# Performance work log

Measured on AMD Instinct MI355X. Metric: run time of the kernel, lower is better.

The kernel has to match this reference:

```python
import jax, jax.numpy as jnp
import numpy as np
from jax import lax

B, S, W = 64, 64, 12          # batch, sentences, words-per-sentence (max_seq)
V, SYM, HID = 32000, 128, 256  # vocab, symbol_size, hidden_size
E, R = 64, 32                  # entity_size, role_size
EPS = 1e-5


def _mlp(x, W1, b1, W2, b2):
    # equation 'b...e,er->b...r' is a matmul on the last axis; tanh hidden, linear out
    return jnp.tanh(x @ W1 + b1) @ W2 + b2


def _ln(x, g, b):
    mu = jnp.mean(x, axis=-1, keepdims=True)
    var = jnp.mean(jnp.square(x - mu), axis=-1, keepdims=True)
    return (x - mu) * lax.rsqrt(var + EPS) * g + b


def setup_inputs() -> dict:
    key = jax.random.key(0)
    ks = jax.random.split(key, 24)
    s_in = 1.0 / np.sqrt(SYM)
    s_h = 1.0 / np.sqrt(HID)
    inp = {
        "story": jax.random.randint(ks[0], (B, S, W), 0, V),
        "query": jax.random.randint(ks[1], (B, W), 0, V),
        "word_embed": jax.random.uniform(ks[2], (V, SYM), jnp.float32, -0.1, 0.1),
        "pos_embed": jnp.ones((W, SYM), jnp.float32) / W,
        # UpdateModule MLPs: 2 entity heads (out=E), 3 role heads (out=R), stacked
        "ue_W1": jax.random.normal(ks[3], (2, SYM, HID)) * s_in,
        "ue_b1": jnp.zeros((2, HID), jnp.float32),
        "ue_W2": jax.random.normal(ks[4], (2, HID, E)) * s_h,
        "ue_b2": jnp.zeros((2, E), jnp.float32),
        "ur_W1": jax.random.normal(ks[5], (3, SYM, HID)) * s_in,
        "ur_b1": jnp.zeros((3, HID), jnp.float32),
        "ur_W2": jax.random.normal(ks[6], (3, HID, R)) * s_h,
        "ur_b2": jnp.zeros((3, R), jnp.float32),
        # InferenceModule MLPs
        "ie_W1": jax.random.normal(ks[7], (2, SYM, HID)) * s_in,
        "ie_b1": jnp.zeros((2, HID), jnp.float32),
        "ie_W2": jax.random.normal(ks[8], (2, HID, E)) * s_h,
        "ie_b2": jnp.zeros((2, E), jnp.float32),
        "ir_W1": jax.random.normal(ks[9], (3, SYM, HID)) * s_in,
        "ir_b1": jnp.zeros((3, HID), jnp.float32),
        "ir_W2": jax.random.normal(ks[10], (3, HID, R)) * s_h,
        "ir_b2": jnp.zeros((3, R), jnp.float32),
        "ln_g": jnp.ones((3, E), jnp.float32),
        "ln_b": jnp.zeros((3, E), jnp.float32),
        "Z": jax.random.normal(ks[11], (E, V)) * (1.0 / np.sqrt(E)),
    }
    return inp


def reference(story, query, word_embed, pos_embed,
              ue_W1, ue_b1, ue_W2, ue_b2, ur_W1, ur_b1, ur_W2, ur_b2,
              ie_W1, ie_b1, ie_W2, ie_b2, ir_W1, ir_b1, ir_W2, ir_b2,
              ln_g, ln_b, Z):
    # ---- InputModule ----
    sent = jnp.einsum('bswe,we->bse', word_embed[story], pos_embed)   # [B,S,SYM]
    qsum = jnp.einsum('bwe,we->be', word_embed[query], pos_embed)     # [B,SYM]

    # ---- UpdateModule: precompute per-step entity/role vectors ----
    e1 = _mlp(sent, ue_W1[0], ue_b1[0], ue_W2[0], ue_b2[0])  # [B,S,E]
    e2 = _mlp(sent, ue_W1[1], ue_b1[1], ue_W2[1], ue_b2[1])
    r1 = _mlp(sent, ur_W1[0], ur_b1[0], ur_W2[0], ur_b2[0])  # [B,S,R]
    r2 = _mlp(sent, ur_W1[1], ur_b1[1], ur_W2[1], ur_b2[1])
    r3 = _mlp(sent, ur_W1[2], ur_b1[2], ur_W2[2], ur_b2[2])
    paW = jnp.einsum('bsr,bsf->bsrf', r1, e2)
    paB = jnp.einsum('bsr,bsf->bsrf', r3, e1)

    xs = tuple(jnp.moveaxis(t, 1, 0) for t in (e1, r1, paW, e2, r2, paB, r3))

    def step(TPR, x):
        e1i, r1i, paWi, e2i, r2i, paBi, r3i = x
        t1 = jnp.einsum('be,berf->brf', e1i, TPR)
        w_hat = jnp.einsum('br,brf->bf', r1i, t1)
        m_hat = jnp.einsum('br,brf->bf', r2i, t1)
        b_hat = jnp.einsum('be,br,berf->bf', e2i, r3i, TPR)
        write_op = paWi - r1i[:, :, None] * w_hat[:, None, :]
        move_op = r2i[:, :, None] * (w_hat - m_hat)[:, None, :]
        back_op = paBi - r3i[:, :, None] * b_hat[:, None, :]
        delta = (jnp.einsum('be,brf->berf', e1i, write_op + move_op)
                 + jnp.einsum('be,brf->berf', e2i, back_op))
        return TPR + delta, None

    TPR0 = jnp.zeros((sent.shape[0], E, R, E), sent.dtype)
    TPR, _ = lax.scan(step, TPR0, xs)

    # ---- InferenceModule ----
    qe1 = _mlp(qsum, ie_W1[0], ie_b1[0], ie_W2[0], ie_b2[0])
    qr1 = _mlp(qsum, ir_W1[0], ir_b1[0], ir_W2[0], ir_b2[0])
    qr2 = _mlp(qsum, ir_W1[1], ir_b1[1], ir_W2[1], ir_b2[1])
    qr3 = _mlp(qsum, ir_W1[2], ir_b1[2], ir_W2[2], ir_b2[2])
    i1 = _ln(jnp.einsum('be,br,berf->bf', qe1, qr1, TPR), ln_g[0], ln_b[0])
    i2 = _ln(jnp.einsum('be,br,berf->bf', i1, qr2, TPR), ln_g[1], ln_b[1])
    i3 = _ln(jnp.einsum('be,br,berf->bf', i2, qr3, TPR), ln_g[2], ln_b[2])
    return (i1 + i2 + i3) @ Z
```

## Files before the change

### kernel.cpp

```cpp
#include <hip/hip_runtime.h>
#include <math.h>

#define B_   64
#define S_   64
#define W_   12
#define V_   32000
#define SYM_ 128
#define HID_ 256
#define E_   64
#define R_   32

__global__ __launch_bounds__(128) void k_embed(
    const int* __restrict__ story, const int* __restrict__ query,
    const float* __restrict__ we, const float* __restrict__ pe,
    float* __restrict__ X) {
  int row = blockIdx.x;
  int e = threadIdx.x;
  const int* idx = (row < 4096) ? story + row * W_ : query + (row - 4096) * W_;
  float acc = 0.f;
#pragma unroll
  for (int w = 0; w < W_; ++w)
    acc = fmaf(we[(long)idx[w] * SYM_ + e], pe[w * SYM_ + e], acc);
  X[row * SYM_ + e] = acc;
}

__global__ __launch_bounds__(256) void k_mlp(
    const float* __restrict__ X,
    const float* __restrict__ ueW1, const float* __restrict__ ueb1,
    const float* __restrict__ ueW2, const float* __restrict__ ueb2,
    const float* __restrict__ urW1, const float* __restrict__ urb1,
    const float* __restrict__ urW2, const float* __restrict__ urb2,
    const float* __restrict__ ieW1, const float* __restrict__ ieb1,
    const float* __restrict__ ieW2, const float* __restrict__ ieb2,
    const float* __restrict__ irW1, const float* __restrict__ irb1,
    const float* __restrict__ irW2, const float* __restrict__ irb2,
    float* __restrict__ oE0, float* __restrict__ oE1,
    float* __restrict__ oR0, float* __restrict__ oR1, float* __restrict__ oR2) {
  __shared__ float SM[8320];

  int h = blockIdx.x % 5;
  int tile = blockIdx.x / 5;
  int rowbase = tile * 32;
  bool isQ = (rowbase >= 4096);
  bool isE = (h < 2);
  const float* W1 = isE ? (isQ ? ieW1 : ueW1) + h * (SYM_ * HID_)
                        : (isQ ? irW1 : urW1) + (h - 2) * (SYM_ * HID_);
  const float* b1 = isE ? (isQ ? ieb1 : ueb1) + h * HID_
                        : (isQ ? irb1 : urb1) + (h - 2) * HID_;
  const float* W2 = isE ? (isQ ? ieW2 : ueW2) + h * (HID_ * E_)
                        : (isQ ? irW2 : urW2) + (h - 2) * (HID_ * R_);
  const float* b2 = isE ? (isQ ? ieb2 : ueb2) + h * E_
                        : (isQ ? irb2 : urb2) + (h - 2) * R_;
  float* out = (h == 0) ? oE0 : (h == 1) ? oE1 : (h == 2) ? oR0 : (h == 3) ? oR1 : oR2;

  int tid = threadIdx.x;
  int wv = tid >> 6;
  int l = tid & 63;

#pragma unroll
  for (int c = 0; c < 4; ++c) {
    int i = tid + 256 * c;
    int row = i >> 5, k4 = (i & 31) * 4;
    *(float4*)&SM[row * 136 + k4] = *(const float4*)(X + (long)(rowbase + row) * SYM_ + k4);
  }
  __syncthreads();

  float a[8][4];
#pragma unroll
  for (int i = 0; i < 8; ++i)
#pragma unroll
    for (int q = 0; q < 4; ++q) a[i][q] = 0.f;

  const float* W1p = W1 + 4 * l;
#pragma unroll 2
  for (int kg = 0; kg < 32; ++kg) {
    float4 w0 = *(const float4*)(W1p + (long)(4 * kg + 0) * HID_);
    float4 w1 = *(const float4*)(W1p + (long)(4 * kg + 1) * HID_);
    float4 w2 = *(const float4*)(W1p + (long)(4 * kg + 2) * HID_);
    float4 w3 = *(const float4*)(W1p + (long)(4 * kg + 3) * HID_);
    float4 xr[8];
#pragma unroll
    for (int i = 0; i < 8; ++i)
      xr[i] = *(const float4*)&SM[(8 * wv + i) * 136 + 4 * kg];
#pragma unroll
    for (int i = 0; i < 8; ++i) {
      a[i][0] = fmaf(xr[i].x, w0.x, a[i][0]);
      a[i][1] = fmaf(xr[i].x, w0.y, a[i][1]);
      a[i][2] = fmaf(xr[i].x, w0.z, a[i][2]);
      a[i][3] = fmaf(xr[i].x, w0.w, a[i][3]);
      a[i][0] = fmaf(xr[i].y, w1.x, a[i][0]);
      a[i][1] = fmaf(xr[i].y, w1.y, a[i][1]);
      a[i][2] = fmaf(xr[i].y, w1.z, a[i][2]);
      a[i][3] = fmaf(xr[i].y, w1.w, a[i][3]);
      a[i][0] = fmaf(xr[i].z, w2.x, a[i][0]);
      a[i][1] = fmaf(xr[i].z, w2.y, a[i][1]);
      a[i][2] = fmaf(xr[i].z, w2.z, a[i][2]);
      a[i][3] = fmaf(xr[i].z, w2.w, a[i][3]);
      a[i][0] = fmaf(xr[i].w, w3.x, a[i][0]);
      a[i][1] = fmaf(xr[i].w, w3.y, a[i][1]);
      a[i][2] = fmaf(xr[i].w, w3.z, a[i][2]);
      a[i][3] = fmaf(xr[i].w, w3.w, a[i][3]);
    }
  }
  __syncthreads();
  {
    float4 b1v = *(const float4*)(b1 + 4 * l);
#pragma unroll
    for (int i = 0; i < 8; ++i) {
      float4 hv = make_float4(tanhf(a[i][0] + b1v.x), tanhf(a[i][1] + b1v.y),
                              tanhf(a[i][2] + b1v.z), tanhf(a[i][3] + b1v.w));
      *(float4*)&SM[(8 * wv + i) * 260 + 4 * l] = hv;
    }
  }
  __syncthreads();
  if (isE) {
    float acc[8];
#pragma unroll
    for (int i = 0; i < 8; ++i) acc[i] = 0.f;
#pragma unroll 2
    for (int c4 = 0; c4 < 64; ++c4) {
      float w0 = W2[(long)(4 * c4 + 0) * E_ + l];
      float w1 = W2[(long)(4 * c4 + 1) * E_ + l];
      float w2 = W2[(long)(4 * c4 + 2) * E_ + l];
      float w3 = W2[(long)(4 * c4 + 3) * E_ + l];
#pragma unroll
      for (int i = 0; i < 8; ++i) {
        float4 hh = *(const float4*)&SM[(8 * wv + i) * 260 + 4 * c4];
        acc[i] = fmaf(hh.x, w0, fmaf(hh.y, w1, fmaf(hh.z, w2, fmaf(hh.w, w3, acc[i]))));
      }
    }
    float bb = b2[l];
#pragma unroll
    for (int i = 0; i < 8; ++i)
      out[(long)(rowbase + 8 * wv + i) * E_ + l] = acc[i] + bb;
  } else {
    int lc = l & 31;
    float acc[8];
#pragma unroll
    for (int i = 0; i < 8; ++i) acc[i] = 0.f;
#pragma unroll 2
    for (int c4 = 0; c4 < 64; ++c4) {
      float w0 = W2[(long)(4 * c4 + 0) * R_ + lc];
      float w1 = W2[(long)(4 * c4 + 1) * R_ + lc];
      float w2 = W2[(long)(4 * c4 + 2) * R_ + lc];
      float w3 = W2[(long)(4 * c4 + 3) * R_ + lc];
#pragma unroll
      for (int i = 0; i < 8; ++i) {
        float4 hh = *(const float4*)&SM[(8 * wv + i) * 260 + 4 * c4];
        acc[i] = fmaf(hh.x, w0, fmaf(hh.y, w1, fmaf(hh.z, w2, fmaf(hh.w, w3, acc[i]))));
      }
    }
    if (l < 32) {
      float bb = b2[lc];
#pragma unroll
      for (int i = 0; i < 8; ++i)
        out[(long)(rowbase + 8 * wv + i) * R_ + lc] = acc[i] + bb;
    }
  }
}

__global__ __launch_bounds__(256) void k_gram(
    const float* __restrict__ e1, const float* __restrict__ e2,
    const float* __restrict__ r1, const float* __restrict__ r2,
    const float* __restrict__ r3, float* __restrict__ Wt) {
  int b = blockIdx.x / 9, m = blockIdx.x % 9;
  const float* sE = ((m < 6) ? e1 : e2) + (long)b * S_ * E_;
  const float* jE = ((m == 2 || m == 5 || m == 8) ? e2 : e1) + (long)b * S_ * E_;
  int sk = m / 3, jk = m % 3;
  const float* sR = ((sk == 0) ? r1 : (sk == 1) ? r2 : r3) + (long)b * S_ * R_;
  const float* jR = ((jk == 0) ? r1 : (jk == 1) ? r2 : r3) + (long)b * S_ * R_;

  __shared__ float Es[64][68], Ej[64][68], Rs[64][36], Rj[64][36];
  int tid = threadIdx.x;
  for (int i = tid; i < 1024; i += 256) {
    int row = i >> 4, c = i & 15;
    *(float4*)&Es[row][4 * c] = *(const float4*)(sE + row * 64 + 4 * c);
    *(float4*)&Ej[row][4 * c] = *(const float4*)(jE + row * 64 + 4 * c);
  }
  for (int i = tid; i < 512; i += 256) {
    int row = i >> 3, c = i & 7;
    *(float4*)&Rs[row][4 * c] = *(const float4*)(sR + row * 32 + 4 * c);
    *(float4*)&Rj[row][4 * c] = *(const float4*)(jR + row * 32 + 4 * c);
  }
  __syncthreads();

  int s0 = (tid & 15) * 4, j0 = (tid >> 4) * 4;
  float ed[4][4] = {}, rd[4][4] = {};
#pragma unroll 4
  for (int k = 0; k < 16; ++k) {
    float4 es[4], ej[4];
#pragma unroll
    for (int i = 0; i < 4; ++i) {
      es[i] = *(const float4*)&Es[s0 + i][4 * k];
      ej[i] = *(const float4*)&Ej[j0 + i][4 * k];
    }
#pragma unroll
    for (int i = 0; i < 4; ++i)
#pragma unroll
      for (int j = 0; j < 4; ++j)
        ed[i][j] = fmaf(es[i].x, ej[j].x, fmaf(es[i].y, ej[j].y,
                   fmaf(es[i].z, ej[j].z, fmaf(es[i].w, ej[j].w, ed[i][j]))));
  }
#pragma unroll 4
  for (int k = 0; k < 8; ++k) {
    float4 rs[4], rj[4];
#pragma unroll
    for (int i = 0; i < 4; ++i) {
      rs[i] = *(const float4*)&Rs[s0 + i][4 * k];
      rj[i] = *(const float4*)&Rj[j0 + i][4 * k];
    }
#pragma unroll
    for (int i = 0; i < 4; ++i)
#pragma unroll
      for (int j = 0; j < 4; ++j)
        rd[i][j] = fmaf(rs[i].x, rj[j].x, fmaf(rs[i].y, rj[j].y,
                   fmaf(rs[i].z, rj[j].z, fmaf(rs[i].w, rj[j].w, rd[i][j]))));
  }
  float* wout = Wt + (long)(b * 9 + m) * 4096;
#pragma unroll
  for (int jj = 0; jj < 4; ++jj) {
    float4 o4 = make_float4(ed[0][jj] * rd[0][jj], ed[1][jj] * rd[1][jj],
                            ed[2][jj] * rd[2][jj], ed[3][jj] * rd[3][jj]);
    *(float4*)(wout + (j0 + jj) * 64 + s0) = o4;
  }
}

__global__ __launch_bounds__(256) void k_scan(
    const float* __restrict__ e1g, const float* __restrict__ e2g,
    const float* __restrict__ Wt, float4* __restrict__ acd) {
  __shared__ float WtL[9 * 512];
  int b = blockIdx.x & 63;
  int g = blockIdx.x >> 6;
  int tid = threadIdx.x;
  int wv = tid >> 6;
  int lane = tid & 63;
  int f0 = g * 8 + wv * 2;
  int f1 = f0 + 1;
  const float* Wb = Wt + (long)b * 9 * 4096;
  long eoff = ((long)b * 64 + lane) * 64;
  float e1x = e1g[eoff + f0], e1y = e1g[eoff + f1];
  float e2x = e2g[eoff + f0], e2y = e2g[eoff + f1];

  float pW0 = 0.f, pM0 = 0.f, pB0 = 0.f;
  float pW1 = 0.f, pM1 = 0.f, pB1 = 0.f;
  float ca0 = e2x, cc0 = 0.f, cd0 = e1x;
  float ca1 = e2y, cc1 = 0.f, cd1 = e1y;
  float ka0 = 0.f, kc0 = 0.f, kd0 = 0.f;
  float ka1 = 0.f, kc1 = 0.f, kd1 = 0.f;

  for (int jc = 0; jc < 8; ++jc) {
    __syncthreads();
    for (int i = tid; i < 1152; i += 256) {
      int m = i >> 7;
      int off = (i & 127) * 4;
      *(float4*)&WtL[m * 512 + off] = *(const float4*)(Wb + m * 4096 + jc * 512 + off);
    }
    __syncthreads();
#pragma unroll
    for (int jj = 0; jj < 8; ++jj) {
      int j = jc * 8 + jj;
      float wa = WtL[0 * 512 + jj * 64 + lane];
      float wc = WtL[1 * 512 + jj * 64 + lane];
      float wd = WtL[2 * 512 + jj * 64 + lane];
      float ma = WtL[3 * 512 + jj * 64 + lane];
      float mc = WtL[4 * 512 + jj * 64 + lane];
      float md = WtL[5 * 512 + jj * 64 + lane];
      float ba = WtL[6 * 512 + jj * 64 + lane];
      float bc = WtL[7 * 512 + jj * 64 + lane];
      float bd = WtL[8 * 512 + jj * 64 + lane];
      float aj0 = __int_as_float(__builtin_amdgcn_readlane(__float_as_int(ca0), j));
      float cj0 = __int_as_float(__builtin_amdgcn_readlane(__float_as_int(cc0), j));
      float dj0 = __int_as_float(__builtin_amdgcn_readlane(__float_as_int(cd0), j));
      float aj1 = __int_as_float(__builtin_amdgcn_readlane(__float_as_int(ca1), j));
      float cj1 = __int_as_float(__builtin_amdgcn_readlane(__float_as_int(cc1), j));
      float dj1 = __int_as_float(__builtin_amdgcn_readlane(__float_as_int(cd1), j));
      bool own = (lane == j);
      ka0 = own ? ca0 : ka0; kc0 = own ? cc0 : kc0; kd0 = own ? cd0 : kd0;
      ka1 = own ? ca1 : ka1; kc1 = own ? cc1 : kc1; kd1 = own ? cd1 : kd1;
      pW0 = fmaf(wa, aj0, pW0); pW0 = fmaf(wc, cj0, pW0); pW0 = fmaf(wd, dj0, pW0);
      pM0 = fmaf(ma, aj0, pM0); pM0 = fmaf(mc, cj0, pM0); pM0 = fmaf(md, dj0, pM0);
      pB0 = fmaf(ba, aj0, pB0); pB0 = fmaf(bc, cj0, pB0); pB0 = fmaf(bd, dj0, pB0);
      pW1 = fmaf(wa, aj1, pW1); pW1 = fmaf(wc, cj1, pW1); pW1 = fmaf(wd, dj1, pW1);
      pM1 = fmaf(ma, aj1, pM1); pM1 = fmaf(mc, cj1, pM1); pM1 = fmaf(md, dj1, pM1);
      pB1 = fmaf(ba, aj1, pB1); pB1 = fmaf(bc, cj1, pB1); pB1 = fmaf(bd, dj1, pB1);
      ca0 = e2x - pW0; cc0 = pW0 - pM0; cd0 = e1x - pB0;
      ca1 = e2y - pW1; cc1 = pW1 - pM1; cd1 = e1y - pB1;
    }
  }
  acd[eoff + f0] = make_float4(ka0, kc0, kd0, 0.f);
  acd[eoff + f1] = make_float4(ka1, kc1, kd1, 0.f);
}

__global__ __launch_bounds__(1024) void k_infer(
    const float4* __restrict__ acd,
    const float* __restrict__ e1, const float* __restrict__ e2,
    const float* __restrict__ r1, const float* __restrict__ r2,
    const float* __restrict__ r3,
    const float* __restrict__ qe1, const float* __restrict__ qr1,
    const float* __restrict__ qr2, const float* __restrict__ qr3,
    const float* __restrict__ lng, const float* __restrict__ lnb,
    float* __restrict__ isum) {
  int b = blockIdx.x, tid = threadIdx.x;
  __shared__ float hista[64 * 65], histc[64 * 65], histd[64 * 65];
  __shared__ float vlds[9 * 64];
  __shared__ float ivec[64];
  __shared__ float u1s[64], u2s[64];
  __shared__ float dsc[64];

  {
    const float4* ab = acd + (long)b * 4096;
    for (int idx = tid; idx < 4096; idx += 1024) {
      float4 hv = ab[idx];
      int j = idx >> 6, f = idx & 63;
      hista[j * 65 + f] = hv.x;
      histc[j * 65 + f] = hv.y;
      histd[j * 65 + f] = hv.z;
    }
  }
  if (tid < 576) {
    int pk = tid >> 6, j = tid & 63;
    int p = pk / 3, k = pk % 3;
    const float* rv = ((k == 0) ? r1 : (k == 1) ? r2 : r3) + ((long)b * 64 + j) * 32;
    const float* q = ((p == 0) ? qr1 : (p == 1) ? qr2 : qr3) + b * 32;
    float acc = 0.f;
#pragma unroll
    for (int t = 0; t < 8; ++t) {
      float4 rv4 = *(const float4*)(rv + 4 * t);
      float4 q4 = *(const float4*)(q + 4 * t);
      acc = fmaf(rv4.x, q4.x, fmaf(rv4.y, q4.y,
            fmaf(rv4.z, q4.z, fmaf(rv4.w, q4.w, acc))));
    }
    vlds[pk * 64 + j] = acc;
  }
  if (tid < 64) ivec[tid] = qe1[b * 64 + tid];
  __syncthreads();

  int f = tid >> 4, jsl = tid & 15;
  int dotd = tid >> 3, dt = tid & 7;
  int which = dotd >> 6, dj = dotd & 63;
  const float* erow = (which ? e2 : e1) + ((long)b * 64 + dj) * 64 + dt * 8;
  float isacc = 0.f;
  for (int p = 0; p < 3; ++p) {
    {
      float acc = 0.f;
#pragma unroll
      for (int t = 0; t < 8; ++t)
        acc = fmaf(erow[t], ivec[dt * 8 + t], acc);
      acc += __shfl_xor(acc, 1, 64);
      acc += __shfl_xor(acc, 2, 64);
      acc += __shfl_xor(acc, 4, 64);
      if (dt == 0) { if (which) u2s[dj] = acc; else u1s[dj] = acc; }
    }
    __syncthreads();
    float part = 0.f;
#pragma unroll
    for (int i = 0; i < 4; ++i) {
      int j = jsl * 4 + i;
      float ca = u1s[j] * vlds[(p * 3 + 0) * 64 + j];
      float cc = u1s[j] * vlds[(p * 3 + 1) * 64 + j];
      float cd = u2s[j] * vlds[(p * 3 + 2) * 64 + j];
      part = fmaf(ca, hista[j * 65 + f],
             fmaf(cc, histc[j * 65 + f],
             fmaf(cd, histd[j * 65 + f], part)));
    }
    part += __shfl_xor(part, 1, 64);
    part += __shfl_xor(part, 2, 64);
    part += __shfl_xor(part, 4, 64);
    part += __shfl_xor(part, 8, 64);
    if (jsl == 0) dsc[f] = part;
    __syncthreads();
    if (tid < 64) {
      float v = dsc[tid];
      float mu = v;
#pragma unroll
      for (int mm = 1; mm <= 32; mm <<= 1) mu += __shfl_xor(mu, mm, 64);
      mu *= (1.f / 64.f);
      float d = v - mu;
      float vr = d * d;
#pragma unroll
      for (int mm = 1; mm <= 32; mm <<= 1) vr += __shfl_xor(vr, mm, 64);
      vr *= (1.f / 64.f);
      float iv = d * (1.f / sqrtf(vr + 1e-5f)) * lng[p * 64 + tid] + lnb[p * 64 + tid];
      ivec[tid] = iv;
      isacc += iv;
    }
    __syncthreads();
  }
  if (tid < 64) isum[b * 64 + tid] = isacc;
}

__global__ __launch_bounds__(256) void k_final(
    const float* __restrict__ isum, const float* __restrict__ Zm,
    float* __restrict__ out) {
  __shared__ float isT[64 * 68];
  int tid = threadIdx.x;
  for (int i = tid; i < 4096; i += 256) {
    int bb = i >> 6, e = i & 63;
    isT[e * 68 + bb] = isum[i];
  }
  __syncthreads();
  int tr = tid >> 4, tc = tid & 15;
  int v0 = blockIdx.x * 64 + tc * 4;
  float acc[4][4] = {};
#pragma unroll 2
  for (int e = 0; e < 64; ++e) {
    float4 a4 = *(const float4*)&isT[e * 68 + 4 * tr];
    float4 z4 = *(const float4*)(Zm + (long)e * V_ + v0);
    float as[4] = {a4.x, a4.y, a4.z, a4.w};
    float zs[4] = {z4.x, z4.y, z4.z, z4.w};
#pragma unroll
    for (int i = 0; i < 4; ++i)
#pragma unroll
      for (int j = 0; j < 4; ++j) acc[i][j] = fmaf(as[i], zs[j], acc[i][j]);
  }
#pragma unroll
  for (int i = 0; i < 4; ++i) {
    float4 o4 = make_float4(acc[i][0], acc[i][1], acc[i][2], acc[i][3]);
    *(float4*)(out + (long)(4 * tr + i) * V_ + v0) = o4;
  }
}

extern "C" void kernel_launch(void* const* d_in, const int* in_sizes, int n_in,
                              void* d_out, int out_size, void* d_ws, size_t ws_size,
                              hipStream_t stream) {
  const int* story = (const int*)d_in[0];
  const int* query = (const int*)d_in[1];
  const float* we = (const float*)d_in[2];
  const float* pe = (const float*)d_in[3];
  const float* ueW1 = (const float*)d_in[4];
  const float* ueb1 = (const float*)d_in[5];
  const float* ueW2 = (const float*)d_in[6];
  const float* ueb2 = (const float*)d_in[7];
  const float* urW1 = (const float*)d_in[8];
  const float* urb1 = (const float*)d_in[9];
  const float* urW2 = (const float*)d_in[10];
  const float* urb2 = (const float*)d_in[11];
  const float* ieW1 = (const float*)d_in[12];
  const float* ieb1 = (const float*)d_in[13];
  const float* ieW2 = (const float*)d_in[14];
  const float* ieb2 = (const float*)d_in[15];
  const float* irW1 = (const float*)d_in[16];
  const float* irb1 = (const float*)d_in[17];
  const float* irW2 = (const float*)d_in[18];
  const float* irb2 = (const float*)d_in[19];
  const float* lng = (const float*)d_in[20];
  const float* lnb = (const float*)d_in[21];
  const float* Zm = (const float*)d_in[22];

  float* ws = (float*)d_ws;
  float* X = ws;
  float* e1 = X + 532480;
  float* e2 = e1 + 266240;
  float* r1 = e2 + 266240;
  float* r2 = r1 + 133120;
  float* r3 = r2 + 133120;
  float* isum = r3 + 133120;
  float* Wt = isum + 4096;
  float4* acd = (float4*)(Wt + 2359296);
  float* qe1 = e1 + 4096 * 64;
  float* qr1 = r1 + 4096 * 32;
  float* qr2 = r2 + 4096 * 32;
  float* qr3 = r3 + 4096 * 32;
  float* outF = (float*)d_out;

  k_embed<<<4160, 128, 0, stream>>>(story, query, we, pe, X);
  k_mlp<<<130 * 5, 256, 0, stream>>>(X, ueW1, ueb1, ueW2, ueb2,
                                     urW1, urb1, urW2, urb2,
                                     ieW1, ieb1, ieW2, ieb2,
                                     irW1, irb1, irW2, irb2,
                                     e1, e2, r1, r2, r3);
  k_gram<<<64 * 9, 256, 0, stream>>>(e1, e2, r1, r2, r3, Wt);
  k_scan<<<512, 256, 0, stream>>>(e1, e2, Wt, acd);
  k_infer<<<B_, 1024, 0, stream>>>(acd, e1, e2, r1, r2, r3, qe1, qr1, qr2, qr3,
                                   lng, lnb, isum);
  k_final<<<V_ / 64, 256, 0, stream>>>(isum, Zm, outF);
}
```

Before: 225.5 us.

## Make MLP kernel wave-private with fast tanh and split-K role head

Gives each wavefront its own shared-memory slice: each wave loads only its own 8 input rows, and the block-wide barriers become per-wave LDS waitcnt fences. Replaces tanhf with an exp/rcp-based approximation. The role-head second layer now splits the hidden dimension between the two wave halves and combines them with a cross-lane shuffle, so no lanes do duplicate work. This cuts barrier stalls and redundant FMAs, at some cost in tanh accuracy and with a reliance on the wave-local fence being enough for LDS visibility.

```diff
diff --git a/kernel.cpp b/kernel.cpp
--- a/kernel.cpp
+++ b/kernel.cpp
@@ -9,6 +9,13 @@
 #define HID_ 256
 #define E_   64
 #define R_   32
+
+#define WAVE_FENCE() asm volatile("s_waitcnt lgkmcnt(0)" ::: "memory")
+
+__device__ __forceinline__ float fast_tanh(float x) {
+  float e = __expf(2.0f * x);
+  return 1.0f - 2.0f * __builtin_amdgcn_rcpf(e + 1.0f);
+}
 
 __global__ __launch_bounds__(128) void k_embed(
     const int* __restrict__ story, const int* __restrict__ query,
@@ -36,7 +43,7 @@
     const float* __restrict__ irW2, const float* __restrict__ irb2,
     float* __restrict__ oE0, float* __restrict__ oE1,
     float* __restrict__ oR0, float* __restrict__ oR1, float* __restrict__ oR2) {
-  __shared__ float SM[8320];
+  __shared__ float SM[4 * 2080];
 
   int h = blockIdx.x % 5;
   int tile = blockIdx.x / 5;
@@ -56,14 +63,16 @@
   int tid = threadIdx.x;
   int wv = tid >> 6;
   int l = tid & 63;
+  float* WS = SM + wv * 2080;
 
 #pragma unroll
   for (int c = 0; c < 4; ++c) {
-    int i = tid + 256 * c;
+    int i = l + 64 * c;
     int row = i >> 5, k4 = (i & 31) * 4;
-    *(float4*)&SM[row * 136 + k4] = *(const float4*)(X + (long)(rowbase + row) * SYM_ + k4);
-  }
-  __syncthreads();
+    *(float4*)&WS[row * 136 + k4] =
+        *(const float4*)(X + (long)(rowbase + 8 * wv + row) * SYM_ + k4);
+  }
+  WAVE_FENCE();
 
   float a[8][4];
 #pragma unroll
@@ -81,7 +90,7 @@
     float4 xr[8];
 #pragma unroll
     for (int i = 0; i < 8; ++i)
-      xr[i] = *(const float4*)&SM[(8 * wv + i) * 136 + 4 * kg];
+      xr[i] = *(const float4*)&WS[i * 136 + 4 * kg];
 #pragma unroll
     for (int i = 0; i < 8; ++i) {
       a[i][0] = fmaf(xr[i].x, w0.x, a[i][0]);
@@ -102,17 +111,17 @@
       a[i][3] = fmaf(xr[i].w, w3.w, a[i][3]);
     }
   }
-  __syncthreads();
   {
     float4 b1v = *(const float4*)(b1 + 4 * l);
 #pragma unroll
     for (int i = 0; i < 8; ++i) {
-      float4 hv = make_float4(tanhf(a[i][0] + b1v.x), tanhf(a[i][1] + b1v.y),
-                              tanhf(a[i][2] + b1v.z), tanhf(a[i][3] + b1v.w));
-      *(float4*)&SM[(8 * wv + i) * 260 + 4 * l] = hv;
-    }
-  }
-  __syncthreads();
+      float4 hv = make_float4(fast_tanh(a[i][0] + b1v.x), fast_tanh(a[i][1] + b1v.y),
+                              fast_tanh(a[i][2] + b1v.z), fast_tanh(a[i][3] + b1v.w));
+      *(float4*)&WS[i * 260 + 4 * l] = hv;
+    }
+  }
+  WAVE_FENCE();
+
   if (isE) {
     float acc[8];
 #pragma unroll
@@ -125,7 +134,7 @@
       float w3 = W2[(long)(4 * c4 + 3) * E_ + l];
 #pragma unroll
       for (int i = 0; i < 8; ++i) {
-        float4 hh = *(const float4*)&SM[(8 * wv + i) * 260 + 4 * c4];
+        float4 hh = *(const float4*)&WS[i * 260 + 4 * c4];
         acc[i] = fmaf(hh.x, w0, fmaf(hh.y, w1, fmaf(hh.z, w2, fmaf(hh.w, w3, acc[i]))));
       }
     }
@@ -135,21 +144,25 @@
       out[(long)(rowbase + 8 * wv + i) * E_ + l] = acc[i] + bb;
   } else {
     int lc = l & 31;
+    int c4base = (l >> 5) * 32;
     float acc[8];
 #pragma unroll
     for (int i = 0; i < 8; ++i) acc[i] = 0.f;
 #pragma unroll 2
-    for (int c4 = 0; c4 < 64; ++c4) {
+    for (int c4o = 0; c4o < 32; ++c4o) {
+      int c4 = c4base + c4o;
       float w0 = W2[(long)(4 * c4 + 0) * R_ + lc];
       float w1 = W2[(long)(4 * c4 + 1) * R_ + lc];
       float w2 = W2[(long)(4 * c4 + 2) * R_ + lc];
       float w3 = W2[(long)(4 * c4 + 3) * R_ + lc];
 #pragma unroll
       for (int i = 0; i < 8; ++i) {
-        float4 hh = *(const float4*)&SM[(8 * wv + i) * 260 + 4 * c4];
+        float4 hh = *(const float4*)&WS[i * 260 + 4 * c4];
         acc[i] = fmaf(hh.x, w0, fmaf(hh.y, w1, fmaf(hh.z, w2, fmaf(hh.w, w3, acc[i]))));
       }
     }
+#pragma unroll
+    for (int i = 0; i < 8; ++i) acc[i] += __shfl_xor(acc[i], 32, 64);
     if (l < 32) {
       float bb = b2[lc];
 #pragma unroll
```

Measured after the change: 215.4 us. 4.5% less time.

## Restructure MLP kernel to single-wave blocks with register broadcasts and fast tanh

Applied to the files above, without the earlier changes.

The MLP kernel moves from 256-thread blocks handling 32 rows to 64-thread single-wavefront blocks handling 8 rows. That gives four times as many blocks and removes shared memory and __syncthreads. Inputs and hidden activations stay in registers and are broadcast across lanes with readlane instead of being staged through LDS. tanhf is replaced with an exp/rcp approximation. Each block now reloads W1/W2 for fewer rows, and the many scalar readlane operations may add instruction overhead.

```diff
diff --git a/kernel.cpp b/kernel.cpp
--- a/kernel.cpp
+++ b/kernel.cpp
@@ -10,6 +10,15 @@
 #define E_   64
 #define R_   32
 
+__device__ __forceinline__ float fast_tanh(float x) {
+  float e = __expf(2.0f * x);
+  return 1.0f - 2.0f * __builtin_amdgcn_rcpf(e + 1.0f);
+}
+
+__device__ __forceinline__ float bcast(float v, int lane) {
+  return __int_as_float(__builtin_amdgcn_readlane(__float_as_int(v), lane));
+}
+
 __global__ __launch_bounds__(128) void k_embed(
     const int* __restrict__ story, const int* __restrict__ query,
     const float* __restrict__ we, const float* __restrict__ pe,
@@ -24,7 +33,7 @@
   X[row * SYM_ + e] = acc;
 }
 
-__global__ __launch_bounds__(256) void k_mlp(
+__global__ __launch_bounds__(64) void k_mlp(
     const float* __restrict__ X,
     const float* __restrict__ ueW1, const float* __restrict__ ueb1,
     const float* __restrict__ ueW2, const float* __restrict__ ueb2,
@@ -36,11 +45,8 @@
     const float* __restrict__ irW2, const float* __restrict__ irb2,
     float* __restrict__ oE0, float* __restrict__ oE1,
     float* __restrict__ oR0, float* __restrict__ oR1, float* __restrict__ oR2) {
-  __shared__ float SM[8320];
-
   int h = blockIdx.x % 5;
-  int tile = blockIdx.x / 5;
-  int rowbase = tile * 32;
+  int rowbase = (blockIdx.x / 5) * 8;
   bool isQ = (rowbase >= 4096);
   bool isE = (h < 2);
   const float* W1 = isE ? (isQ ? ieW1 : ueW1) + h * (SYM_ * HID_)
@@ -53,23 +59,18 @@
                         : (isQ ? irb2 : urb2) + (h - 2) * R_;
   float* out = (h == 0) ? oE0 : (h == 1) ? oE1 : (h == 2) ? oR0 : (h == 3) ? oR1 : oR2;
 
-  int tid = threadIdx.x;
-  int wv = tid >> 6;
-  int l = tid & 63;
-
-#pragma unroll
-  for (int c = 0; c < 4; ++c) {
-    int i = tid + 256 * c;
-    int row = i >> 5, k4 = (i & 31) * 4;
-    *(float4*)&SM[row * 136 + k4] = *(const float4*)(X + (long)(rowbase + row) * SYM_ + k4);
-  }
-  __syncthreads();
+  int l = threadIdx.x;
+
+  float2 xreg[8];
+#pragma unroll
+  for (int r = 0; r < 8; ++r)
+    xreg[r] = *(const float2*)(X + (long)(rowbase + r) * SYM_ + 2 * l);
 
   float a[8][4];
 #pragma unroll
-  for (int i = 0; i < 8; ++i)
-#pragma unroll
-    for (int q = 0; q < 4; ++q) a[i][q] = 0.f;
+  for (int r = 0; r < 8; ++r)
+#pragma unroll
+    for (int q = 0; q < 4; ++q) a[r][q] = 0.f;
 
   const float* W1p = W1 + 4 * l;
 #pragma unroll 2
@@ -78,83 +79,91 @@
     float4 w1 = *(const float4*)(W1p + (long)(4 * kg + 1) * HID_);
     float4 w2 = *(const float4*)(W1p + (long)(4 * kg + 2) * HID_);
     float4 w3 = *(const float4*)(W1p + (long)(4 * kg + 3) * HID_);
-    float4 xr[8];
-#pragma unroll
-    for (int i = 0; i < 8; ++i)
-      xr[i] = *(const float4*)&SM[(8 * wv + i) * 136 + 4 * kg];
-#pragma unroll
-    for (int i = 0; i < 8; ++i) {
-      a[i][0] = fmaf(xr[i].x, w0.x, a[i][0]);
-      a[i][1] = fmaf(xr[i].x, w0.y, a[i][1]);
-      a[i][2] = fmaf(xr[i].x, w0.z, a[i][2]);
-      a[i][3] = fmaf(xr[i].x, w0.w, a[i][3]);
-      a[i][0] = fmaf(xr[i].y, w1.x, a[i][0]);
-      a[i][1] = fmaf(xr[i].y, w1.y, a[i][1]);
-      a[i][2] = fmaf(xr[i].y, w1.z, a[i][2]);
-      a[i][3] = fmaf(xr[i].y, w1.w, a[i][3]);
-      a[i][0] = fmaf(xr[i].z, w2.x, a[i][0]);
-      a[i][1] = fmaf(xr[i].z, w2.y, a[i][1]);
-      a[i][2] = fmaf(xr[i].z, w2.z, a[i][2]);
-      a[i][3] = fmaf(xr[i].z, w2.w, a[i][3]);
-      a[i][0] = fmaf(xr[i].w, w3.x, a[i][0]);
-      a[i][1] = fmaf(xr[i].w, w3.y, a[i][1]);
-      a[i][2] = fmaf(xr[i].w, w3.z, a[i][2]);
-      a[i][3] = fmaf(xr[i].w, w3.w, a[i][3]);
-    }
-  }
-  __syncthreads();
+    int la = 2 * kg, lb = 2 * kg + 1;
+#pragma unroll
+    for (int r = 0; r < 8; ++r) {
+      float x0 = bcast(xreg[r].x, la);
+      float x1 = bcast(xreg[r].y, la);
+      float x2 = bcast(xreg[r].x, lb);
+      float x3 = bcast(xreg[r].y, lb);
+      a[r][0] = fmaf(x0, w0.x, a[r][0]);
+      a[r][1] = fmaf(x0, w0.y, a[r][1]);
+      a[r][2] = fmaf(x0, w0.z, a[r][2]);
+      a[r][3] = fmaf(x0, w0.w, a[r][3]);
+      a[r][0] = fmaf(x1, w1.x, a[r][0]);
+      a[r][1] = fmaf(x1, w1.y, a[r][1]);
+      a[r][2] = fmaf(x1, w1.z, a[r][2]);
+      a[r][3] = fmaf(x1, w1.w, a[r][3]);
+      a[r][0] = fmaf(x2, w2.x, a[r][0]);
+      a[r][1] = fmaf(x2, w2.y, a[r][1]);
+      a[r][2] = fmaf(x2, w2.z, a[r][2]);
+      a[r][3] = fmaf(x2, w2.w, a[r][3]);
+      a[r][0] = fmaf(x3, w3.x, a[r][0]);
+      a[r][1] = fmaf(x3, w3.y, a[r][1]);
+      a[r][2] = fmaf(x3, w3.z, a[r][2]);
+      a[r][3] = fmaf(x3, w3.w, a[r][3]);
+    }
+  }
+
   {
     float4 b1v = *(const float4*)(b1 + 4 * l);
 #pragma unroll
-    for (int i = 0; i < 8; ++i) {
-      float4 hv = make_float4(tanhf(a[i][0] + b1v.x), tanhf(a[i][1] + b1v.y),
-                              tanhf(a[i][2] + b1v.z), tanhf(a[i][3] + b1v.w));
-      *(float4*)&SM[(8 * wv + i) * 260 + 4 * l] = hv;
-    }
-  }
-  __syncthreads();
+    for (int r = 0; r < 8; ++r) {
+      a[r][0] = fast_tanh(a[r][0] + b1v.x);
+      a[r][1] = fast_tanh(a[r][1] + b1v.y);
+      a[r][2] = fast_tanh(a[r][2] + b1v.z);
+      a[r][3] = fast_tanh(a[r][3] + b1v.w);
+    }
+  }
+
   if (isE) {
     float acc[8];
 #pragma unroll
-    for (int i = 0; i < 8; ++i) acc[i] = 0.f;
+    for (int r = 0; r < 8; ++r) acc[r] = 0.f;
 #pragma unroll 2
-    for (int c4 = 0; c4 < 64; ++c4) {
-      float w0 = W2[(long)(4 * c4 + 0) * E_ + l];
-      float w1 = W2[(long)(4 * c4 + 1) * E_ + l];
-      float w2 = W2[(long)(4 * c4 + 2) * E_ + l];
-      float w3 = W2[(long)(4 * c4 + 3) * E_ + l];
-#pragma unroll
-      for (int i = 0; i < 8; ++i) {
-        float4 hh = *(const float4*)&SM[(8 * wv + i) * 260 + 4 * c4];
-        acc[i] = fmaf(hh.x, w0, fmaf(hh.y, w1, fmaf(hh.z, w2, fmaf(hh.w, w3, acc[i]))));
+    for (int g = 0; g < 64; ++g) {
+      float w0 = W2[(long)(4 * g + 0) * E_ + l];
+      float w1 = W2[(long)(4 * g + 1) * E_ + l];
+      float w2 = W2[(long)(4 * g + 2) * E_ + l];
+      float w3 = W2[(long)(4 * g + 3) * E_ + l];
+#pragma unroll
+      for (int r = 0; r < 8; ++r) {
+        float h0 = bcast(a[r][0], g);
+        float h1 = bcast(a[r][1], g);
+        float h2 = bcast(a[r][2], g);
+        float h3 = bcast(a[r][3], g);
+        acc[r] = fmaf(h0, w0, fmaf(h1, w1, fmaf(h2, w2, fmaf(h3, w3, acc[r]))));
       }
     }
     float bb = b2[l];
 #pragma unroll
-    for (int i = 0; i < 8; ++i)
-      out[(long)(rowbase + 8 * wv + i) * E_ + l] = acc[i] + bb;
+    for (int r = 0; r < 8; ++r)
+      out[(long)(rowbase + r) * E_ + l] = acc[r] + bb;
   } else {
     int lc = l & 31;
     float acc[8];
 #pragma unroll
-    for (int i = 0; i < 8; ++i) acc[i] = 0.f;
+    for (int r = 0; r < 8; ++r) acc[r] = 0.f;
 #pragma unroll 2
-    for (int c4 = 0; c4 < 64; ++c4) {
-      float w0 = W2[(long)(4 * c4 + 0) * R_ + lc];
-      float w1 = W2[(long)(4 * c4 + 1) * R_ + lc];
-      float w2 = W2[(long)(4 * c4 + 2) * R_ + lc];
-      float w3 = W2[(long)(4 * c4 + 3) * R_ + lc];
-#pragma unroll
-      for (int i = 0; i < 8; ++i) {
-        float4 hh = *(const float4*)&SM[(8 * wv + i) * 260 + 4 * c4];
-        acc[i] = fmaf(hh.x, w0, fmaf(hh.y, w1, fmaf(hh.z, w2, fmaf(hh.w, w3, acc[i]))));
+    for (int g = 0; g < 64; ++g) {
+      float w0 = W2[(long)(4 * g + 0) * R_ + lc];
+      float w1 = W2[(long)(4 * g + 1) * R_ + lc];
+      float w2 = W2[(long)(4 * g + 2) * R_ + lc];
+      float w3 = W2[(long)(4 * g + 3) * R_ + lc];
+#pragma unroll
+      for (int r = 0; r < 8; ++r) {
+        float h0 = bcast(a[r][0], g);
+        float h1 = bcast(a[r][1], g);
+        float h2 = bcast(a[r][2], g);
+        float h3 = bcast(a[r][3], g);
+        acc[r] = fmaf(h0, w0, fmaf(h1, w1, fmaf(h2, w2, fmaf(h3, w3, acc[r]))));
       }
     }
     if (l < 32) {
       float bb = b2[lc];
 #pragma unroll
-      for (int i = 0; i < 8; ++i)
-        out[(long)(rowbase + 8 * wv + i) * R_ + lc] = acc[i] + bb;
+      for (int r = 0; r < 8; ++r)
+        out[(long)(rowbase + r) * R_ + lc] = acc[r] + bb;
     }
   }
 }
@@ -464,11 +473,11 @@
   float* outF = (float*)d_out;
 
   k_embed<<<4160, 128, 0, stream>>>(story, query, we, pe, X);
-  k_mlp<<<130 * 5, 256, 0, stream>>>(X, ueW1, ueb1, ueW2, ueb2,
-                                     urW1, urb1, urW2, urb2,
-                                     ieW1, ieb1, ieW2, ieb2,
-                                     irW1, irb1, irW2, irb2,
-                                     e1, e2, r1, r2, r3);
+  k_mlp<<<520 * 5, 64, 0, stream>>>(X, ueW1, ueb1, ueW2, ueb2,
+                                    urW1, urb1, urW2, urb2,
+                                    ieW1, ieb1, ieW2, ieb2,
+                                    irW1, irb1, irW2, irb2,
+                                    e1, e2, r1, r2, r3);
   k_gram<<<64 * 9, 256, 0, stream>>>(e1, e2, r1, r2, r3, Wt);
   k_scan<<<512, 256, 0, stream>>>(e1, e2, Wt, acd);
   k_infer<<<B_, 1024, 0, stream>>>(acd, e1, e2, r1, r2, r3, qe1, qr1, qr2, qr3,
```

Measured after the change: 255.4 us. +13.2%, slower.

## Move MLP matmuls to bf16x3 split MFMA with prepacked weight fragments

Applied to the files above, without the earlier changes.

Replaces the scalar FP32 FMA MLP with MFMA 16x16x32 bf16 instructions. Each FP32 operand is split into bf16 hi and lo parts and three products are accumulated to keep near-FP32 accuracy. A new k_wprep kernel repacks and splits the weights into the MFMA fragment layout inside the Wt workspace, which k_gram later overwrites. tanhf is swapped for an exp/rcp approximation. The aim is to cut the MLP's ALU-bound time, at the cost of an extra launch, reduced precision and a faster but less exact tanh.

```diff
diff --git a/kernel.cpp b/kernel.cpp
--- a/kernel.cpp
+++ b/kernel.cpp
@@ -10,6 +10,35 @@
 #define E_   64
 #define R_   32
 
+typedef short bf16x8 __attribute__((ext_vector_type(8)));
+typedef float f32x4 __attribute__((ext_vector_type(4)));
+#define MFMA16 __builtin_amdgcn_mfma_f32_16x16x32_bf16
+
+__device__ __forceinline__ float fast_tanh(float x) {
+  float e = __expf(2.0f * x);
+  return 1.0f - 2.0f * __builtin_amdgcn_rcpf(e + 1.0f);
+}
+
+__device__ __forceinline__ void split1(float x, unsigned short& h, unsigned short& l) {
+  unsigned u = __float_as_uint(x);
+  h = (unsigned short)(u >> 16);
+  float r = x - __uint_as_float(u & 0xFFFF0000u);
+  unsigned v = __float_as_uint(r);
+  l = (unsigned short)((v + 0x7FFFu + ((v >> 16) & 1u)) >> 16);
+}
+
+__device__ __forceinline__ void split8(const float4& a, const float4& b,
+                                       bf16x8& h8, bf16x8& l8) {
+  float xs[8] = {a.x, a.y, a.z, a.w, b.x, b.y, b.z, b.w};
+#pragma unroll
+  for (int j = 0; j < 8; ++j) {
+    unsigned short hh, ll;
+    split1(xs[j], hh, ll);
+    h8[j] = (short)hh;
+    l8[j] = (short)ll;
+  }
+}
+
 __global__ __launch_bounds__(128) void k_embed(
     const int* __restrict__ story, const int* __restrict__ query,
     const float* __restrict__ we, const float* __restrict__ pe,
@@ -24,138 +53,193 @@
   X[row * SYM_ + e] = acc;
 }
 
+__global__ __launch_bounds__(64) void k_wprep(
+    const float* __restrict__ ueW1, const float* __restrict__ urW1,
+    const float* __restrict__ ieW1, const float* __restrict__ irW1,
+    const float* __restrict__ ueW2, const float* __restrict__ urW2,
+    const float* __restrict__ ieW2, const float* __restrict__ irW2,
+    unsigned short* __restrict__ w1ph, unsigned short* __restrict__ w1pl,
+    unsigned short* __restrict__ w2ph, unsigned short* __restrict__ w2pl) {
+  int l = threadIdx.x;
+  int bid = blockIdx.x;
+  bf16x8 h8, l8;
+  if (bid < 640) {
+    int slot = bid >> 6, rem = bid & 63;
+    int nt = rem >> 2, ks = rem & 3;
+    int grp = slot / 5, h = slot % 5;
+    const float* src = (h < 2) ? ((grp ? ieW1 : ueW1) + h * (SYM_ * HID_))
+                               : ((grp ? irW1 : urW1) + (h - 2) * (SYM_ * HID_));
+    int kk = ks * 32 + (l >> 4) * 8;
+    int n = nt * 16 + (l & 15);
+#pragma unroll
+    for (int j = 0; j < 8; ++j) {
+      unsigned short hh, ll;
+      split1(src[(long)(kk + j) * HID_ + n], hh, ll);
+      h8[j] = (short)hh;
+      l8[j] = (short)ll;
+    }
+    long dst = ((long)(slot * 16 + nt) * 4 + ks) * 512 + l * 8;
+    *(bf16x8*)(w1ph + dst) = h8;
+    *(bf16x8*)(w1pl + dst) = l8;
+  } else {
+    int fid = bid - 640;
+    int slot = fid >> 5, rem = fid & 31;
+    int nt = rem >> 3, ks = rem & 7;
+    int grp = slot / 5, h = slot % 5;
+    bool isE = h < 2;
+    if (!isE && nt >= 2) return;
+    int NC = isE ? E_ : R_;
+    const float* src = isE ? ((grp ? ieW2 : ueW2) + h * (HID_ * E_))
+                           : ((grp ? irW2 : urW2) + (h - 2) * (HID_ * R_));
+    int kk = ks * 32 + (l >> 4) * 8;
+    int n = nt * 16 + (l & 15);
+#pragma unroll
+    for (int j = 0; j < 8; ++j) {
+      unsigned short hh, ll;
+      split1(src[(long)(kk + j) * NC + n], hh, ll);
+      h8[j] = (short)hh;
+      l8[j] = (short)ll;
+    }
+    long dst = ((long)(slot * 4 + nt) * 8 + ks) * 512 + l * 8;
+    *(bf16x8*)(w2ph + dst) = h8;
+    *(bf16x8*)(w2pl + dst) = l8;
+  }
+}
+
 __global__ __launch_bounds__(256) void k_mlp(
     const float* __restrict__ X,
-    const float* __restrict__ ueW1, const float* __restrict__ ueb1,
-    const float* __restrict__ ueW2, const float* __restrict__ ueb2,
-    const float* __restrict__ urW1, const float* __restrict__ urb1,
-    const float* __restrict__ urW2, const float* __restrict__ urb2,
-    const float* __restrict__ ieW1, const float* __restrict__ ieb1,
-    const float* __restrict__ ieW2, const float* __restrict__ ieb2,
-    const float* __restrict__ irW1, const float* __restrict__ irb1,
-    const float* __restrict__ irW2, const float* __restrict__ irb2,
+    const unsigned short* __restrict__ w1ph, const unsigned short* __restrict__ w1pl,
+    const unsigned short* __restrict__ w2ph, const unsigned short* __restrict__ w2pl,
+    const float* __restrict__ ueb1, const float* __restrict__ urb1,
+    const float* __restrict__ ieb1, const float* __restrict__ irb1,
+    const float* __restrict__ ueb2, const float* __restrict__ urb2,
+    const float* __restrict__ ieb2, const float* __restrict__ irb2,
     float* __restrict__ oE0, float* __restrict__ oE1,
     float* __restrict__ oR0, float* __restrict__ oR1, float* __restrict__ oR2) {
-  __shared__ float SM[8320];
+  __shared__ unsigned short Hhi[32][264];
+  __shared__ unsigned short Hlo[32][264];
 
   int h = blockIdx.x % 5;
   int tile = blockIdx.x / 5;
   int rowbase = tile * 32;
-  bool isQ = (rowbase >= 4096);
+  int grp = (rowbase >= 4096) ? 1 : 0;
   bool isE = (h < 2);
-  const float* W1 = isE ? (isQ ? ieW1 : ueW1) + h * (SYM_ * HID_)
-                        : (isQ ? irW1 : urW1) + (h - 2) * (SYM_ * HID_);
-  const float* b1 = isE ? (isQ ? ieb1 : ueb1) + h * HID_
-                        : (isQ ? irb1 : urb1) + (h - 2) * HID_;
-  const float* W2 = isE ? (isQ ? ieW2 : ueW2) + h * (HID_ * E_)
-                        : (isQ ? irW2 : urW2) + (h - 2) * (HID_ * R_);
-  const float* b2 = isE ? (isQ ? ieb2 : ueb2) + h * E_
-                        : (isQ ? irb2 : urb2) + (h - 2) * R_;
+  int slot = grp * 5 + h;
+  const float* b1 = isE ? ((grp ? ieb1 : ueb1) + h * HID_)
+                        : ((grp ? irb1 : urb1) + (h - 2) * HID_);
+  const float* b2 = isE ? ((grp ? ieb2 : ueb2) + h * E_)
+                        : ((grp ? irb2 : urb2) + (h - 2) * R_);
   float* out = (h == 0) ? oE0 : (h == 1) ? oE1 : (h == 2) ? oR0 : (h == 3) ? oR1 : oR2;
 
   int tid = threadIdx.x;
-  int wv = tid >> 6;
+  int w = tid >> 6;
   int l = tid & 63;
-
-#pragma unroll
-  for (int c = 0; c < 4; ++c) {
-    int i = tid + 256 * c;
-    int row = i >> 5, k4 = (i & 31) * 4;
-    *(float4*)&SM[row * 136 + k4] = *(const float4*)(X + (long)(rowbase + row) * SYM_ + k4);
+  int lr = l & 15;
+  int lk = l >> 4;
+
+  f32x4 acc[2][4];
+#pragma unroll
+  for (int mt = 0; mt < 2; ++mt)
+#pragma unroll
+    for (int ntl = 0; ntl < 4; ++ntl) acc[mt][ntl] = (f32x4){0.f, 0.f, 0.f, 0.f};
+
+  const unsigned short* w1hS = w1ph + (long)slot * 32768 + l * 8;
+  const unsigned short* w1lS = w1pl + (long)slot * 32768 + l * 8;
+
+#pragma unroll
+  for (int ks = 0; ks < 4; ++ks) {
+    bf16x8 ah[2], al[2];
+#pragma unroll
+    for (int mt = 0; mt < 2; ++mt) {
+      const float* xp = X + (long)(rowbase + mt * 16 + lr) * SYM_ + ks * 32 + lk * 8;
+      float4 x0 = *(const float4*)xp;
+      float4 x1 = *(const float4*)(xp + 4);
+      split8(x0, x1, ah[mt], al[mt]);
+    }
+#pragma unroll
+    for (int ntl = 0; ntl < 4; ++ntl) {
+      int nt = 4 * w + ntl;
+      long fo = ((long)nt * 4 + ks) * 512;
+      bf16x8 bh = *(const bf16x8*)(w1hS + fo);
+      bf16x8 bl = *(const bf16x8*)(w1lS + fo);
+#pragma unroll
+      for (int mt = 0; mt < 2; ++mt) {
+        acc[mt][ntl] = MFMA16(ah[mt], bh, acc[mt][ntl], 0, 0, 0);
+        acc[mt][ntl] = MFMA16(ah[mt], bl, acc[mt][ntl], 0, 0, 0);
+        acc[mt][ntl] = MFMA16(al[mt], bh, acc[mt][ntl], 0, 0, 0);
+      }
+    }
+  }
+
+#pragma unroll
+  for (int ntl = 0; ntl < 4; ++ntl) {
+    int col = (4 * w + ntl) * 16 + lr;
+    float bb = b1[col];
+#pragma unroll
+    for (int mt = 0; mt < 2; ++mt)
+#pragma unroll
+      for (int reg = 0; reg < 4; ++reg) {
+        float t = fast_tanh(acc[mt][ntl][reg] + bb);
+        unsigned short hh, ll;
+        split1(t, hh, ll);
+        int row = mt * 16 + lk * 4 + reg;
+        Hhi[row][col] = hh;
+        Hlo[row][col] = ll;
+      }
   }
   __syncthreads();
 
-  float a[8][4];
-#pragma unroll
-  for (int i = 0; i < 8; ++i)
-#pragma unroll
-    for (int q = 0; q < 4; ++q) a[i][q] = 0.f;
-
-  const float* W1p = W1 + 4 * l;
-#pragma unroll 2
-  for (int kg = 0; kg < 32; ++kg) {
-    float4 w0 = *(const float4*)(W1p + (long)(4 * kg + 0) * HID_);
-    float4 w1 = *(const float4*)(W1p + (long)(4 * kg + 1) * HID_);
-    float4 w2 = *(const float4*)(W1p + (long)(4 * kg + 2) * HID_);
-    float4 w3 = *(const float4*)(W1p + (long)(4 * kg + 3) * HID_);
-    float4 xr[8];
-#pragma unroll
-    for (int i = 0; i < 8; ++i)
-      xr[i] = *(const float4*)&SM[(8 * wv + i) * 136 + 4 * kg];
-#pragma unroll
-    for (int i = 0; i < 8; ++i) {
-      a[i][0] = fmaf(xr[i].x, w0.x, a[i][0]);
-      a[i][1] = fmaf(xr[i].x, w0.y, a[i][1]);
-      a[i][2] = fmaf(xr[i].x, w0.z, a[i][2]);
-      a[i][3] = fmaf(xr[i].x, w0.w, a[i][3]);
-      a[i][0] = fmaf(xr[i].y, w1.x, a[i][0]);
-      a[i][1] = fmaf(xr[i].y, w1.y, a[i][1]);
-      a[i][2] = fmaf(xr[i].y, w1.z, a[i][2]);
-      a[i][3] = fmaf(xr[i].y, w1.w, a[i][3]);
-      a[i][0] = fmaf(xr[i].z, w2.x, a[i][0]);
-      a[i][1] = fmaf(xr[i].z, w2.y, a[i][1]);
-      a[i][2] = fmaf(xr[i].z, w2.z, a[i][2]);
-      a[i][3] = fmaf(xr[i].z, w2.w, a[i][3]);
-      a[i][0] = fmaf(xr[i].w, w3.x, a[i][0]);
-      a[i][1] = fmaf(xr[i].w, w3.y, a[i][1]);
-      a[i][2] = fmaf(xr[i].w, w3.z, a[i][2]);
-      a[i][3] = fmaf(xr[i].w, w3.w, a[i][3]);
-    }
-  }
-  __syncthreads();
-  {
-    float4 b1v = *(const float4*)(b1 + 4 * l);
-#pragma unroll
-    for (int i = 0; i < 8; ++i) {
-      float4 hv = make_float4(tanhf(a[i][0] + b1v.x), tanhf(a[i][1] + b1v.y),
-                              tanhf(a[i][2] + b1v.z), tanhf(a[i][3] + b1v.w));
-      *(float4*)&SM[(8 * wv + i) * 260 + 4 * l] = hv;
-    }
-  }
-  __syncthreads();
   if (isE) {
-    float acc[8];
-#pragma unroll
-    for (int i = 0; i < 8; ++i) acc[i] = 0.f;
-#pragma unroll 2
-    for (int c4 = 0; c4 < 64; ++c4) {
-      float w0 = W2[(long)(4 * c4 + 0) * E_ + l];
-      float w1 = W2[(long)(4 * c4 + 1) * E_ + l];
-      float w2 = W2[(long)(4 * c4 + 2) * E_ + l];
-      float w3 = W2[(long)(4 * c4 + 3) * E_ + l];
-#pragma unroll
-      for (int i = 0; i < 8; ++i) {
-        float4 hh = *(const float4*)&SM[(8 * wv + i) * 260 + 4 * c4];
-        acc[i] = fmaf(hh.x, w0, fmaf(hh.y, w1, fmaf(hh.z, w2, fmaf(hh.w, w3, acc[i]))));
+    const unsigned short* w2hS = w2ph + (long)slot * 16384 + l * 8;
+    const unsigned short* w2lS = w2pl + (long)slot * 16384 + l * 8;
+    int nt2 = w;
+    f32x4 acc2[2];
+    acc2[0] = (f32x4){0.f, 0.f, 0.f, 0.f};
+    acc2[1] = (f32x4){0.f, 0.f, 0.f, 0.f};
+#pragma unroll
+    for (int ks2 = 0; ks2 < 8; ++ks2) {
+      long fo = ((long)nt2 * 8 + ks2) * 512;
+      bf16x8 bh = *(const bf16x8*)(w2hS + fo);
+      bf16x8 bl = *(const bf16x8*)(w2lS + fo);
+#pragma unroll
+      for (int mt = 0; mt < 2; ++mt) {
+        int row = mt * 16 + lr, kh = ks2 * 32 + lk * 8;
+        bf16x8 ah2 = *(const bf16x8*)&Hhi[row][kh];
+        bf16x8 al2 = *(const bf16x8*)&Hlo[row][kh];
+        acc2[mt] = MFMA16(ah2, bh, acc2[mt], 0, 0, 0);
+        acc2[mt] = MFMA16(ah2, bl, acc2[mt], 0, 0, 0);
+        acc2[mt] = MFMA16(al2, bh, acc2[mt], 0, 0, 0);
       }
     }
-    float bb = b2[l];
-#pragma unroll
-    for (int i = 0; i < 8; ++i)
-      out[(long)(rowbase + 8 * wv + i) * E_ + l] = acc[i] + bb;
+    int col2 = nt2 * 16 + lr;
+    float bb2 = b2[col2];
+#pragma unroll
+    for (int mt = 0; mt < 2; ++mt)
+#pragma unroll
+      for (int reg = 0; reg < 4; ++reg)
+        out[(long)(rowbase + mt * 16 + lk * 4 + reg) * E_ + col2] = acc2[mt][reg] + bb2;
   } else {
-    int lc = l & 31;
-    float acc[8];
-#pragma unroll
-    for (int i = 0; i < 8; ++i) acc[i] = 0.f;
-#pragma unroll 2
-    for (int c4 = 0; c4 < 64; ++c4) {
-      float w0 = W2[(long)(4 * c4 + 0) * R_ + lc];
-      float w1 = W2[(long)(4 * c4 + 1) * R_ + lc];
-      float w2 = W2[(long)(4 * c4 + 2) * R_ + lc];
-      float w3 = W2[(long)(4 * c4 + 3) * R_ + lc];
-#pragma unroll
-      for (int i = 0; i < 8; ++i) {
-        float4 hh = *(const float4*)&SM[(8 * wv + i) * 260 + 4 * c4];
-        acc[i] = fmaf(hh.x, w0, fmaf(hh.y, w1, fmaf(hh.z, w2, fmaf(hh.w, w3, acc[i]))));
-      }
-    }
-    if (l < 32) {
-      float bb = b2[lc];
-#pragma unroll
-      for (int i = 0; i < 8; ++i)
-        out[(long)(rowbase + 8 * wv + i) * R_ + lc] = acc[i] + bb;
-    }
+    const unsigned short* w2hS = w2ph + (long)slot * 16384 + l * 8;
+    const unsigned short* w2lS = w2pl + (long)slot * 16384 + l * 8;
+    int mt = w >> 1, nt2 = w & 1;
+    f32x4 acc2 = (f32x4){0.f, 0.f, 0.f, 0.f};
+#pragma unroll
+    for (int ks2 = 0; ks2 < 8; ++ks2) {
+      long fo = ((long)nt2 * 8 + ks2) * 512;
+      bf16x8 bh = *(const bf16x8*)(w2hS + fo);
+      bf16x8 bl = *(const bf16x8*)(w2lS + fo);
+      int row = mt * 16 + lr, kh = ks2 * 32 + lk * 8;
+      bf16x8 ah2 = *(const bf16x8*)&Hhi[row][kh];
+      bf16x8 al2 = *(const bf16x8*)&Hlo[row][kh];
+      acc2 = MFMA16(ah2, bh, acc2, 0, 0, 0);
+      acc2 = MFMA16(ah2, bl, acc2, 0, 0, 0);
+      acc2 = MFMA16(al2, bh, acc2, 0, 0, 0);
+    }
+    int col2 = nt2 * 16 + lr;
+    float bb2 = b2[col2];
+#pragma unroll
+    for (int reg = 0; reg < 4; ++reg)
+      out[(long)(rowbase + mt * 16 + lk * 4 + reg) * R_ + col2] = acc2[reg] + bb2;
   }
 }
 
@@ -463,11 +547,17 @@
   float* qr3 = r3 + 4096 * 32;
   float* outF = (float*)d_out;
 
+  unsigned short* w1ph = (unsigned short*)Wt;
+  unsigned short* w1pl = w1ph + 327680;
+  unsigned short* w2ph = w1pl + 327680;
+  unsigned short* w2pl = w2ph + 163840;
+
   k_embed<<<4160, 128, 0, stream>>>(story, query, we, pe, X);
-  k_mlp<<<130 * 5, 256, 0, stream>>>(X, ueW1, ueb1, ueW2, ueb2,
-                                     urW1, urb1, urW2, urb2,
-                                     ieW1, ieb1, ieW2, ieb2,
-                                     irW1, irb1, irW2, irb2,
+  k_wprep<<<960, 64, 0, stream>>>(ueW1, urW1, ieW1, irW1, ueW2, urW2, ieW2, irW2,
+                                  w1ph, w1pl, w2ph, w2pl);
+  k_mlp<<<130 * 5, 256, 0, stream>>>(X, w1ph, w1pl, w2ph, w2pl,
+                                     ueb1, urb1, ieb1, irb1,
+                                     ueb2, urb2, ieb2, irb2,
                                      e1, e2, r1, r2, r3);
   k_gram<<<64 * 9, 256, 0, stream>>>(e1, e2, r1, r2, r3, Wt);
   k_scan<<<512, 256, 0, stream>>>(e1, e2, Wt, acd);
```

Result: faster. 197.9 us (-12.3%).
